# Performance work log

Measured on AMD Instinct MI355X. Metric: run time of the kernel, lower is better.

Reference implementation:

```python
import jax, jax.numpy as jnp
import numpy as np

H = 16  # num_heads (matches init_kwargs)
MASK_VAL = -10000.0


def setup_inputs() -> dict:
    key = jax.random.key(0)
    k1, k2, k3, k4, k5 = jax.random.split(key, 5)
    B, N, C = 2, 2048, 1024
    hidden_states = jax.random.normal(k1, (B, N, C), dtype=jnp.float32)
    encoder_hidden_states = jax.random.normal(k2, (B, N, C), dtype=jnp.float32)
    pad_mask = jax.random.bernoulli(k3, 0.1, (B, N))
    # Linear weights stored as (in, out); scaled ~Xavier so softmax isn't saturated
    W_q = jax.random.normal(k4, (C, C), dtype=jnp.float32) * (C ** -0.5)
    W_c = jax.random.normal(k5, (C, 2 * C), dtype=jnp.float32) * (C ** -0.5)
    return {"hidden_states": hidden_states,
            "encoder_hidden_states": encoder_hidden_states,
            "pad_mask": pad_mask,
            "W_q": W_q,
            "W_c": W_c}


def _split_heads(x, B, N, C):
    # (B, N, C) -> (B, H, N, D)
    return x.reshape(B, N, H, C // H).transpose(0, 2, 1, 3)


def reference(hidden_states, encoder_hidden_states, pad_mask, W_q, W_c):
    B, N, C = hidden_states.shape
    D = C // H
    scaler = D ** -0.5

    q = hidden_states @ W_q                       # (B, N, C)
    kv = encoder_hidden_states @ W_c              # (B, N, 2C)
    k, v = kv[..., :C], kv[..., C:]

    q = _split_heads(q, B, N, C)                  # (B, H, N, D)
    k = _split_heads(k, B, N, C)
    v = _split_heads(v, B, N, C)

    scores = jnp.einsum('bhid,bhjd->bhij', q, k) * scaler  # (B, H, N, N)

    # construct_mask: expanded[b,i,j] = pad_mask[b,i] OR pad_mask[b,j]
    expanded = pad_mask[:, None, :, None] | pad_mask[:, None, None, :]
    scores = jnp.where(expanded, MASK_VAL, scores)

    # max-subtract + softmax (dropout_rate=0 so dropout is identity)
    scores = scores - jax.lax.stop_gradient(scores.max(axis=-1, keepdims=True))
    att_weights = jax.nn.softmax(scores, axis=-1)

    att = jnp.einsum('bhij,bhjd->bhid', att_weights, v)   # (B, H, N, D)
    att = att.transpose(0, 2, 1, 3).reshape(B, N, C)
    return att, att_weights
```

## Files before the change

### kernel.cpp

```cpp
#include <hip/hip_runtime.h>
#include <math.h>

#define B_ 2
#define N_ 2048
#define C_ 1024
#define H_ 16
#define D_ 64

typedef __attribute__((ext_vector_type(8))) short short8v;
typedef __attribute__((ext_vector_type(4))) short short4v;
typedef __attribute__((ext_vector_type(4))) float f32x4;

static __device__ __forceinline__ short f2bf(float f) {
    union { float f; unsigned u; } v; v.f = f;
    unsigned r = v.u + 0x7FFFu + ((v.u >> 16) & 1u);
    return (short)(r >> 16);
}

static __device__ __forceinline__ void splitbf(float f, short& h, short& l) {
    union { float f; unsigned u; } v; v.f = f;
    const unsigned uh = v.u & 0xFFFF0000u;
    h = (short)(uh >> 16);
    union { unsigned u; float f; } w; w.u = uh;
    union { float f; unsigned u; } x; x.f = f - w.f;
    l = (short)(x.u >> 16);
}

static __device__ __forceinline__ void lds_barrier() {
    __builtin_amdgcn_sched_barrier(0);
    asm volatile("s_waitcnt lgkmcnt(0)" ::: "memory");
    __builtin_amdgcn_s_barrier();
    __builtin_amdgcn_sched_barrier(0);
}

__global__ __launch_bounds__(256) void split_aw(const float* __restrict__ src,
                                                short* __restrict__ hi,
                                                short* __restrict__ lo,
                                                int nA,
                                                const float* __restrict__ Wm,
                                                short* __restrict__ th,
                                                short* __restrict__ tl,
                                                int K, int N) {
    __shared__ float Ls[64][68];
    const int t = threadIdx.x;
    if ((int)blockIdx.x < nA) {
        const int i = (blockIdx.x * 256 + t) * 4;
        const float4 f = *(const float4*)&src[i];
        short4v h, l;
        short th_, tl_;
        splitbf(f.x, th_, tl_); h[0] = th_; l[0] = tl_;
        splitbf(f.y, th_, tl_); h[1] = th_; l[1] = tl_;
        splitbf(f.z, th_, tl_); h[2] = th_; l[2] = tl_;
        splitbf(f.w, th_, tl_); h[3] = th_; l[3] = tl_;
        *(short4v*)&hi[i] = h;
        *(short4v*)&lo[i] = l;
        return;
    }
    const int wb  = blockIdx.x - nA;
    const int nbx = N / 64;
    const int n0 = (wb % nbx) * 64;
    const int k0 = (wb / nbx) * 64;
#pragma unroll
    for (int it = 0; it < 4; ++it) {
        const int kl = it * 16 + (t >> 4);
        const int nl = (t & 15) * 4;
        *(float4*)&Ls[kl][nl] = *(const float4*)&Wm[(size_t)(k0 + kl) * N + n0 + nl];
    }
    __syncthreads();
#pragma unroll
    for (int it = 0; it < 4; ++it) {
        const int idx = it * 256 + t;
        const int nl  = idx & 63;
        const int ks  = (idx >> 6) * 4;
        short4v h, l;
#pragma unroll
        for (int j = 0; j < 4; ++j) {
            short th_, tl_;
            splitbf(Ls[ks + j][nl], th_, tl_);
            h[j] = th_; l[j] = tl_;
        }
        *(short4v*)&th[(size_t)(n0 + nl) * K + k0 + ks] = h;
        *(short4v*)&tl[(size_t)(n0 + nl) * K + k0 + ks] = l;
    }
}

#define GKSTR 40

__global__ __launch_bounds__(256) void gemm_bf3(const short* __restrict__ Ah,
                                                const short* __restrict__ Al,
                                                const short* __restrict__ Bth,
                                                const short* __restrict__ Btl,
                                                short* __restrict__ Cm,
                                                int K, int N) {
    __shared__ __align__(16) short Ahs[128][GKSTR];
    __shared__ __align__(16) short Als[128][GKSTR];
    __shared__ __align__(16) short Bhs[128][GKSTR];
    __shared__ __align__(16) short Bls[128][GKSTR];

    const int t  = threadIdx.x;
    const int w  = t >> 6;
    const int lq = t & 15;
    const int hq = (t & 63) >> 4;
    const int wr = w >> 1;
    const int wc = w & 1;
    const int m0 = blockIdx.y * 128;
    const int n0 = blockIdx.x * 128;

    const int srow = t >> 1;
    const int scol = (t & 1) * 16;

    const short* gA_h = &Ah[(size_t)(m0 + srow) * K + scol];
    const short* gA_l = &Al[(size_t)(m0 + srow) * K + scol];
    const short* gB_h = &Bth[(size_t)(n0 + srow) * K + scol];
    const short* gB_l = &Btl[(size_t)(n0 + srow) * K + scol];

    f32x4 acc[4][4];
#pragma unroll
    for (int mi = 0; mi < 4; ++mi)
#pragma unroll
        for (int ni = 0; ni < 4; ++ni) acc[mi][ni] = (f32x4){0.f, 0.f, 0.f, 0.f};

    short8v ra_h0 = *(const short8v*)gA_h,       ra_h1 = *(const short8v*)(gA_h + 8);
    short8v ra_l0 = *(const short8v*)gA_l,       ra_l1 = *(const short8v*)(gA_l + 8);
    short8v rb_h0 = *(const short8v*)gB_h,       rb_h1 = *(const short8v*)(gB_h + 8);
    short8v rb_l0 = *(const short8v*)gB_l,       rb_l1 = *(const short8v*)(gB_l + 8);

    for (int k0 = 0; k0 < K; k0 += 32) {
        __syncthreads();
        *(short8v*)&Ahs[srow][scol]     = ra_h0;
        *(short8v*)&Ahs[srow][scol + 8] = ra_h1;
        *(short8v*)&Als[srow][scol]     = ra_l0;
        *(short8v*)&Als[srow][scol + 8] = ra_l1;
        *(short8v*)&Bhs[srow][scol]     = rb_h0;
        *(short8v*)&Bhs[srow][scol + 8] = rb_h1;
        *(short8v*)&Bls[srow][scol]     = rb_l0;
        *(short8v*)&Bls[srow][scol + 8] = rb_l1;
        __syncthreads();

        const int kn = k0 + 32;
        if (kn < K) {
            ra_h0 = *(const short8v*)(gA_h + kn); ra_h1 = *(const short8v*)(gA_h + kn + 8);
            ra_l0 = *(const short8v*)(gA_l + kn); ra_l1 = *(const short8v*)(gA_l + kn + 8);
            rb_h0 = *(const short8v*)(gB_h + kn); rb_h1 = *(const short8v*)(gB_h + kn + 8);
            rb_l0 = *(const short8v*)(gB_l + kn); rb_l1 = *(const short8v*)(gB_l + kn + 8);
        }

        short8v bnh[4], bnl[4];
#pragma unroll
        for (int ni = 0; ni < 4; ++ni) {
            bnh[ni] = *(const short8v*)&Bhs[wc * 64 + ni * 16 + lq][hq * 8];
            bnl[ni] = *(const short8v*)&Bls[wc * 64 + ni * 16 + lq][hq * 8];
        }
#pragma unroll
        for (int mi = 0; mi < 4; ++mi) {
            const short8v amh = *(const short8v*)&Ahs[wr * 64 + mi * 16 + lq][hq * 8];
            const short8v aml = *(const short8v*)&Als[wr * 64 + mi * 16 + lq][hq * 8];
#pragma unroll
            for (int ni = 0; ni < 4; ++ni) {
                acc[mi][ni] = __builtin_amdgcn_mfma_f32_16x16x32_bf16(amh, bnh[ni], acc[mi][ni], 0, 0, 0);
                acc[mi][ni] = __builtin_amdgcn_mfma_f32_16x16x32_bf16(amh, bnl[ni], acc[mi][ni], 0, 0, 0);
                acc[mi][ni] = __builtin_amdgcn_mfma_f32_16x16x32_bf16(aml, bnh[ni], acc[mi][ni], 0, 0, 0);
            }
        }
    }

#pragma unroll
    for (int mi = 0; mi < 4; ++mi)
#pragma unroll
        for (int ni = 0; ni < 4; ++ni) {
            const int col = n0 + wc * 64 + ni * 16 + lq;
#pragma unroll
            for (int r = 0; r < 4; ++r) {
                const int row = m0 + wr * 64 + mi * 16 + hq * 4 + r;
                Cm[(size_t)row * N + col] = f2bf(acc[mi][ni][r]);
            }
        }
}

__global__ __launch_bounds__(256) void v_transpose(const short* __restrict__ kv_bf,
                                                   short* __restrict__ vt) {
    __shared__ __align__(16) short Ls[128][72];
    const int t  = threadIdx.x;
    const int jt = blockIdx.x * 128;
    const int h  = blockIdx.y;
    const int b  = blockIdx.z;
    const short* src = kv_bf + (size_t)b * N_ * 2 * C_ + C_ + h * D_;
#pragma unroll
    for (int it = 0; it < 4; ++it) {
        const int idx = it * 256 + t;
        const int j = idx >> 3, d0 = (idx & 7) * 8;
        *(short8v*)&Ls[j][d0] = *(const short8v*)&src[(size_t)(jt + j) * (2 * C_) + d0];
    }
    __syncthreads();
    short* dst = vt + ((size_t)(b * H_ + h)) * D_ * N_;
#pragma unroll
    for (int it = 0; it < 4; ++it) {
        const int idx = it * 256 + t;
        const int d  = idx >> 4;
        const int j0 = (idx & 15) * 8;
        short8v s;
#pragma unroll
        for (int jj = 0; jj < 8; ++jj) s[jj] = Ls[j0 + jj][d];
        *(short8v*)&dst[(size_t)d * N_ + jt + j0] = s;
    }
}

#define KSTR 72
#define VSTR 136
#define PSTR 136

__global__ __launch_bounds__(256) void attn_mfma(const short* __restrict__ q,
                                                 const short* __restrict__ kv,
                                                 const short* __restrict__ vtg,
                                                 const int* __restrict__ mask,
                                                 float* __restrict__ out_att,
                                                 float* __restrict__ out_w) {
    __shared__ __align__(16) short Ks[128][KSTR];
    __shared__ __align__(16) short Vt[64][VSTR];
    __shared__ __align__(16) short Ps[4][32][PSTR];
    __shared__ float linv_s[4][32];
    __shared__ int   mcol_s[128];

    const int t  = threadIdx.x;
    const int w  = t >> 6;
    const int l  = t & 63;
    const int lq = l & 15;
    const int hq = l >> 4;

    const int lin = blockIdx.x;
    const int swz = (lin & 7) * 64 + (lin >> 3);
    const int qb = swz & 15;
    const int h  = (swz >> 4) & 15;
    const int b  = swz >> 8;
    const int i0 = qb * 128 + w * 32;

    const int sj = t >> 3;
    const int sd = (t & 7) * 8;
    const int vd = t >> 4;
    const int vj = (t & 15) * 8;

    short8v qa[2][2];
#pragma unroll
    for (int g = 0; g < 2; ++g) {
        const short* qrow = q + ((size_t)(b * N_ + i0 + g * 16 + lq)) * C_ + h * D_;
        qa[g][0] = *(const short8v*)&qrow[hq * 8];
        qa[g][1] = *(const short8v*)&qrow[32 + hq * 8];
    }

    int mr[2][4];
#pragma unroll
    for (int g = 0; g < 2; ++g)
#pragma unroll
        for (int r = 0; r < 4; ++r) mr[g][r] = mask[b * N_ + i0 + g * 16 + hq * 4 + r];

    const short* kbase = kv + (size_t)b * N_ * 2 * C_ + h * D_;
    const short* vtb   = vtg + ((size_t)(b * H_ + h)) * D_ * N_;

    float lsum[2][4];
#pragma unroll
    for (int g = 0; g < 2; ++g)
#pragma unroll
        for (int r = 0; r < 4; ++r) lsum[g][r] = 0.f;

    short8v kr[4];
    int mpre = 0;
#pragma unroll
    for (int it = 0; it < 4; ++it)
        kr[it] = *(const short8v*)&kbase[(size_t)(it * 32 + sj) * (2 * C_) + sd];
    if (t < 128) mpre = mask[b * N_ + t];

    for (int tile = 0; tile < 16; ++tile) {
        lds_barrier();
#pragma unroll
        for (int it = 0; it < 4; ++it)
            *(short8v*)&Ks[it * 32 + sj][sd] = kr[it];
        if (t < 128) mcol_s[t] = mpre;
        lds_barrier();

        if (tile < 15) {
            const int jn = (tile + 1) * 128;
#pragma unroll
            for (int it = 0; it < 4; ++it)
                kr[it] = *(const short8v*)&kbase[(size_t)(jn + it * 32 + sj) * (2 * C_) + sd];
            if (t < 128) mpre = mask[b * N_ + jn + t];
        }

#pragma unroll
        for (int cb = 0; cb < 8; ++cb) {
            const short8v b0 = *(short8v*)&Ks[cb * 16 + lq][hq * 8];
            const short8v b1 = *(short8v*)&Ks[cb * 16 + lq][32 + hq * 8];
            const int mc = mcol_s[cb * 16 + lq];
#pragma unroll
            for (int g = 0; g < 2; ++g) {
                f32x4 acc = {0.f, 0.f, 0.f, 0.f};
                acc = __builtin_amdgcn_mfma_f32_16x16x32_bf16(qa[g][0], b0, acc, 0, 0, 0);
                acc = __builtin_amdgcn_mfma_f32_16x16x32_bf16(qa[g][1], b1, acc, 0, 0, 0);
#pragma unroll
                for (int r = 0; r < 4; ++r)
                    lsum[g][r] += mr[g][r] ? 1.0f : (mc ? 0.0f : __expf(acc[r] * 0.125f));
            }
        }
    }
    float inv[2][4];
#pragma unroll
    for (int g = 0; g < 2; ++g)
#pragma unroll
        for (int r = 0; r < 4; ++r) {
            float s = lsum[g][r];
#pragma unroll
            for (int off = 1; off < 16; off <<= 1) s += __shfl_xor(s, off, 64);
            inv[g][r] = 1.0f / s;
        }
    if (lq == 0)
#pragma unroll
        for (int g = 0; g < 2; ++g)
#pragma unroll
            for (int r = 0; r < 4; ++r) linv_s[w][g * 16 + hq * 4 + r] = inv[g][r];

    float* wbase[2];
#pragma unroll
    for (int g = 0; g < 2; ++g)
        wbase[g] = out_w + ((size_t)((b * H_ + h) * N_ + i0 + g * 16 + hq * 4)) * N_;

    f32x4 oacc[4][2];
#pragma unroll
    for (int db = 0; db < 4; ++db)
#pragma unroll
        for (int g = 0; g < 2; ++g) oacc[db][g] = (f32x4){0.f, 0.f, 0.f, 0.f};

    short8v vr[4];
#pragma unroll
    for (int it = 0; it < 4; ++it) {
        kr[it] = *(const short8v*)&kbase[(size_t)(it * 32 + sj) * (2 * C_) + sd];
        vr[it] = *(const short8v*)&vtb[(size_t)(it * 16 + vd) * N_ + vj];
    }
    if (t < 128) mpre = mask[b * N_ + t];

    for (int tile = 0; tile < 16; ++tile) {
        const int jt = tile * 128;
        lds_barrier();
#pragma unroll
        for (int it = 0; it < 4; ++it) {
            *(short8v*)&Ks[it * 32 + sj][sd] = kr[it];
            *(short8v*)&Vt[it * 16 + vd][vj] = vr[it];
        }
        if (t < 128) mcol_s[t] = mpre;
        lds_barrier();

        if (tile < 15) {
            const int jn = jt + 128;
#pragma unroll
            for (int it = 0; it < 4; ++it) {
                kr[it] = *(const short8v*)&kbase[(size_t)(jn + it * 32 + sj) * (2 * C_) + sd];
                vr[it] = *(const short8v*)&vtb[(size_t)(it * 16 + vd) * N_ + jn + vj];
            }
            if (t < 128) mpre = mask[b * N_ + jn + t];
        }

#pragma unroll
        for (int cb = 0; cb < 8; ++cb) {
            const short8v b0 = *(short8v*)&Ks[cb * 16 + lq][hq * 8];
            const short8v b1 = *(short8v*)&Ks[cb * 16 + lq][32 + hq * 8];
            const int mc   = mcol_s[cb * 16 + lq];
            const int jcol = cb * 16 + lq;
#pragma unroll
            for (int g = 0; g < 2; ++g) {
                f32x4 acc = {0.f, 0.f, 0.f, 0.f};
                acc = __builtin_amdgcn_mfma_f32_16x16x32_bf16(qa[g][0], b0, acc, 0, 0, 0);
                acc = __builtin_amdgcn_mfma_f32_16x16x32_bf16(qa[g][1], b1, acc, 0, 0, 0);
#pragma unroll
                for (int r = 0; r < 4; ++r) {
                    const float ev = mr[g][r] ? 1.0f : (mc ? 0.0f : __expf(acc[r] * 0.125f));
                    wbase[g][(size_t)r * N_ + jt + jcol] = ev * inv[g][r];
                    Ps[w][g * 16 + hq * 4 + r][jcol] = f2bf(ev);
                }
            }
        }

        short8v pb[2][4];
#pragma unroll
        for (int kb = 0; kb < 4; ++kb) {
            pb[0][kb] = *(short8v*)&Ps[w][lq][kb * 32 + hq * 8];
            pb[1][kb] = *(short8v*)&Ps[w][16 + lq][kb * 32 + hq * 8];
        }
#pragma unroll
        for (int db = 0; db < 4; ++db)
#pragma unroll
            for (int kb = 0; kb < 4; ++kb) {
                const short8v va = *(short8v*)&Vt[db * 16 + lq][kb * 32 + hq * 8];
                oacc[db][0] = __builtin_amdgcn_mfma_f32_16x16x32_bf16(va, pb[0][kb], oacc[db][0], 0, 0, 0);
                oacc[db][1] = __builtin_amdgcn_mfma_f32_16x16x32_bf16(va, pb[1][kb], oacc[db][1], 0, 0, 0);
            }
    }

#pragma unroll
    for (int g = 0; g < 2; ++g) {
        const float invi = linv_s[w][g * 16 + lq];
        const size_t abase = ((size_t)(b * N_ + i0 + g * 16 + lq)) * C_ + h * D_;
#pragma unroll
        for (int db = 0; db < 4; ++db)
#pragma unroll
            for (int r = 0; r < 4; ++r)
                out_att[abase + db * 16 + hq * 4 + r] = oacc[db][g][r] * invi;
    }
}

extern "C" void kernel_launch(void* const* d_in, const int* in_sizes, int n_in,
                              void* d_out, int out_size, void* d_ws, size_t ws_size,
                              hipStream_t stream) {
    const float* hs   = (const float*)d_in[0];
    const float* ehs  = (const float*)d_in[1];
    const int*   mask = (const int*)d_in[2];
    const float* W_q  = (const float*)d_in[3];
    const float* W_c  = (const float*)d_in[4];

    float* out_att = (float*)d_out;
    float* out_w   = (float*)d_out + (size_t)B_ * N_ * C_;

    const size_t M1 = (size_t)1024 * 1024;
    short* qbf  = (short*)d_ws;
    short* kvbf = qbf + 4 * M1;
    short* Ah   = kvbf + 8 * M1;
    short* Al   = Ah + 4 * M1;
    short* vt   = Ah;
    short* Wth  = Al + 4 * M1;
    short* Wtl  = Wth + 2 * M1;

    const int nAblk = (B_ * N_ * C_) / 1024;

    split_aw<<<dim3(nAblk + (C_ / 64) * (C_ / 64)), 256, 0, stream>>>(
        hs, Ah, Al, nAblk, W_q, Wth, Wtl, C_, C_);
    gemm_bf3<<<dim3(C_ / 128, (B_ * N_) / 128), 256, 0, stream>>>(
        Ah, Al, Wth, Wtl, qbf, C_, C_);

    split_aw<<<dim3(nAblk + ((2 * C_) / 64) * (C_ / 64)), 256, 0, stream>>>(
        ehs, Ah, Al, nAblk, W_c, Wth, Wtl, C_, 2 * C_);
    gemm_bf3<<<dim3((2 * C_) / 128, (B_ * N_) / 128), 256, 0, stream>>>(
        Ah, Al, Wth, Wtl, kvbf, C_, 2 * C_);

    v_transpose<<<dim3(N_ / 128, H_, B_), 256, 0, stream>>>(kvbf, vt);
    attn_mfma<<<dim3(512), 256, 0, stream>>>(
        qbf, kvbf, vt, mask, out_att, out_w);
}
```

Measured before the change: 325.9 us.

## Split attention row-sum pass into separate kernel and shrink GEMM N-tile

The softmax denominator pass, previously computed inside the attention kernel before the output pass, moves to its own kernel with 1024 blocks of 16 rows per wave, writing inverse row sums to workspace that the second kernel reads. The projection GEMM tile shrinks from 128x128 to 128x64, doubling the block count to raise occupancy and wave count on the many CUs. This costs an extra launch, recomputing QK^T in both kernels as before, more global traffic for the B-tile reloads, and less register reuse per GEMM block.

```diff
diff --git a/kernel.cpp b/kernel.cpp
--- a/kernel.cpp
+++ b/kernel.cpp
@@ -94,8 +94,8 @@
                                                 int K, int N) {
     __shared__ __align__(16) short Ahs[128][GKSTR];
     __shared__ __align__(16) short Als[128][GKSTR];
-    __shared__ __align__(16) short Bhs[128][GKSTR];
-    __shared__ __align__(16) short Bls[128][GKSTR];
+    __shared__ __align__(16) short Bhs[64][GKSTR];
+    __shared__ __align__(16) short Bls[64][GKSTR];
 
     const int t  = threadIdx.x;
     const int w  = t >> 6;
@@ -104,26 +104,28 @@
     const int wr = w >> 1;
     const int wc = w & 1;
     const int m0 = blockIdx.y * 128;
-    const int n0 = blockIdx.x * 128;
+    const int n0 = blockIdx.x * 64;
 
     const int srow = t >> 1;
     const int scol = (t & 1) * 16;
+    const int brow = t >> 2;
+    const int bcol = (t & 3) * 8;
 
     const short* gA_h = &Ah[(size_t)(m0 + srow) * K + scol];
     const short* gA_l = &Al[(size_t)(m0 + srow) * K + scol];
-    const short* gB_h = &Bth[(size_t)(n0 + srow) * K + scol];
-    const short* gB_l = &Btl[(size_t)(n0 + srow) * K + scol];
-
-    f32x4 acc[4][4];
+    const short* gB_h = &Bth[(size_t)(n0 + brow) * K + bcol];
+    const short* gB_l = &Btl[(size_t)(n0 + brow) * K + bcol];
+
+    f32x4 acc[4][2];
 #pragma unroll
     for (int mi = 0; mi < 4; ++mi)
 #pragma unroll
-        for (int ni = 0; ni < 4; ++ni) acc[mi][ni] = (f32x4){0.f, 0.f, 0.f, 0.f};
-
-    short8v ra_h0 = *(const short8v*)gA_h,       ra_h1 = *(const short8v*)(gA_h + 8);
-    short8v ra_l0 = *(const short8v*)gA_l,       ra_l1 = *(const short8v*)(gA_l + 8);
-    short8v rb_h0 = *(const short8v*)gB_h,       rb_h1 = *(const short8v*)(gB_h + 8);
-    short8v rb_l0 = *(const short8v*)gB_l,       rb_l1 = *(const short8v*)(gB_l + 8);
+        for (int ni = 0; ni < 2; ++ni) acc[mi][ni] = (f32x4){0.f, 0.f, 0.f, 0.f};
+
+    short8v ra_h0 = *(const short8v*)gA_h,  ra_h1 = *(const short8v*)(gA_h + 8);
+    short8v ra_l0 = *(const short8v*)gA_l,  ra_l1 = *(const short8v*)(gA_l + 8);
+    short8v rb_h  = *(const short8v*)gB_h;
+    short8v rb_l  = *(const short8v*)gB_l;
 
     for (int k0 = 0; k0 < K; k0 += 32) {
         __syncthreads();
@@ -131,32 +133,30 @@
         *(short8v*)&Ahs[srow][scol + 8] = ra_h1;
         *(short8v*)&Als[srow][scol]     = ra_l0;
         *(short8v*)&Als[srow][scol + 8] = ra_l1;
-        *(short8v*)&Bhs[srow][scol]     = rb_h0;
-        *(short8v*)&Bhs[srow][scol + 8] = rb_h1;
-        *(short8v*)&Bls[srow][scol]     = rb_l0;
-        *(short8v*)&Bls[srow][scol + 8] = rb_l1;
+        *(short8v*)&Bhs[brow][bcol]     = rb_h;
+        *(short8v*)&Bls[brow][bcol]     = rb_l;
         __syncthreads();
 
         const int kn = k0 + 32;
         if (kn < K) {
             ra_h0 = *(const short8v*)(gA_h + kn); ra_h1 = *(const short8v*)(gA_h + kn + 8);
             ra_l0 = *(const short8v*)(gA_l + kn); ra_l1 = *(const short8v*)(gA_l + kn + 8);
-            rb_h0 = *(const short8v*)(gB_h + kn); rb_h1 = *(const short8v*)(gB_h + kn + 8);
-            rb_l0 = *(const short8v*)(gB_l + kn); rb_l1 = *(const short8v*)(gB_l + kn + 8);
-        }
-
-        short8v bnh[4], bnl[4];
-#pragma unroll
-        for (int ni = 0; ni < 4; ++ni) {
-            bnh[ni] = *(const short8v*)&Bhs[wc * 64 + ni * 16 + lq][hq * 8];
-            bnl[ni] = *(const short8v*)&Bls[wc * 64 + ni * 16 + lq][hq * 8];
+            rb_h  = *(const short8v*)(gB_h + kn);
+            rb_l  = *(const short8v*)(gB_l + kn);
+        }
+
+        short8v bnh[2], bnl[2];
+#pragma unroll
+        for (int ni = 0; ni < 2; ++ni) {
+            bnh[ni] = *(const short8v*)&Bhs[wc * 32 + ni * 16 + lq][hq * 8];
+            bnl[ni] = *(const short8v*)&Bls[wc * 32 + ni * 16 + lq][hq * 8];
         }
 #pragma unroll
         for (int mi = 0; mi < 4; ++mi) {
             const short8v amh = *(const short8v*)&Ahs[wr * 64 + mi * 16 + lq][hq * 8];
             const short8v aml = *(const short8v*)&Als[wr * 64 + mi * 16 + lq][hq * 8];
 #pragma unroll
-            for (int ni = 0; ni < 4; ++ni) {
+            for (int ni = 0; ni < 2; ++ni) {
                 acc[mi][ni] = __builtin_amdgcn_mfma_f32_16x16x32_bf16(amh, bnh[ni], acc[mi][ni], 0, 0, 0);
                 acc[mi][ni] = __builtin_amdgcn_mfma_f32_16x16x32_bf16(amh, bnl[ni], acc[mi][ni], 0, 0, 0);
                 acc[mi][ni] = __builtin_amdgcn_mfma_f32_16x16x32_bf16(aml, bnh[ni], acc[mi][ni], 0, 0, 0);
@@ -167,8 +167,8 @@
 #pragma unroll
     for (int mi = 0; mi < 4; ++mi)
 #pragma unroll
-        for (int ni = 0; ni < 4; ++ni) {
-            const int col = n0 + wc * 64 + ni * 16 + lq;
+        for (int ni = 0; ni < 2; ++ni) {
+            const int col = n0 + wc * 32 + ni * 16 + lq;
 #pragma unroll
             for (int r = 0; r < 4; ++r) {
                 const int row = m0 + wr * 64 + mi * 16 + hq * 4 + r;
@@ -209,17 +209,99 @@
 #define VSTR 136
 #define PSTR 136
 
-__global__ __launch_bounds__(256) void attn_mfma(const short* __restrict__ q,
-                                                 const short* __restrict__ kv,
-                                                 const short* __restrict__ vtg,
-                                                 const int* __restrict__ mask,
-                                                 float* __restrict__ out_att,
-                                                 float* __restrict__ out_w) {
+__global__ __launch_bounds__(256) void attn_p1(const short* __restrict__ q,
+                                               const short* __restrict__ kv,
+                                               const int* __restrict__ mask,
+                                               float* __restrict__ linv_g) {
+    __shared__ __align__(16) short Ks[128][KSTR];
+    __shared__ int mcol_s[128];
+
+    const int t  = threadIdx.x;
+    const int w  = t >> 6;
+    const int l  = t & 63;
+    const int lq = l & 15;
+    const int hq = l >> 4;
+
+    const int lin = blockIdx.x;
+    const int swz = (lin & 7) * 128 + (lin >> 3);
+    const int qb = swz & 31;
+    const int h  = (swz >> 5) & 15;
+    const int b  = swz >> 9;
+    const int i0 = qb * 64 + w * 16;
+
+    const int sj = t >> 3;
+    const int sd = (t & 7) * 8;
+
+    short8v qa[2];
+    {
+        const short* qrow = q + ((size_t)(b * N_ + i0 + lq)) * C_ + h * D_;
+        qa[0] = *(const short8v*)&qrow[hq * 8];
+        qa[1] = *(const short8v*)&qrow[32 + hq * 8];
+    }
+    int mr[4];
+#pragma unroll
+    for (int r = 0; r < 4; ++r) mr[r] = mask[b * N_ + i0 + hq * 4 + r];
+
+    const short* kbase = kv + (size_t)b * N_ * 2 * C_ + h * D_;
+
+    float lsum[4] = {0.f, 0.f, 0.f, 0.f};
+    short8v kr[4];
+    int mpre = 0;
+#pragma unroll
+    for (int it = 0; it < 4; ++it)
+        kr[it] = *(const short8v*)&kbase[(size_t)(it * 32 + sj) * (2 * C_) + sd];
+    if (t < 128) mpre = mask[b * N_ + t];
+
+    for (int tile = 0; tile < 16; ++tile) {
+        lds_barrier();
+#pragma unroll
+        for (int it = 0; it < 4; ++it)
+            *(short8v*)&Ks[it * 32 + sj][sd] = kr[it];
+        if (t < 128) mcol_s[t] = mpre;
+        lds_barrier();
+
+        if (tile < 15) {
+            const int jn = (tile + 1) * 128;
+#pragma unroll
+            for (int it = 0; it < 4; ++it)
+                kr[it] = *(const short8v*)&kbase[(size_t)(jn + it * 32 + sj) * (2 * C_) + sd];
+            if (t < 128) mpre = mask[b * N_ + jn + t];
+        }
+
+#pragma unroll
+        for (int cb = 0; cb < 8; ++cb) {
+            f32x4 acc = {0.f, 0.f, 0.f, 0.f};
+            const short8v b0 = *(short8v*)&Ks[cb * 16 + lq][hq * 8];
+            const short8v b1 = *(short8v*)&Ks[cb * 16 + lq][32 + hq * 8];
+            acc = __builtin_amdgcn_mfma_f32_16x16x32_bf16(qa[0], b0, acc, 0, 0, 0);
+            acc = __builtin_amdgcn_mfma_f32_16x16x32_bf16(qa[1], b1, acc, 0, 0, 0);
+            const int mc = mcol_s[cb * 16 + lq];
+#pragma unroll
+            for (int r = 0; r < 4; ++r)
+                lsum[r] += mr[r] ? 1.0f : (mc ? 0.0f : __expf(acc[r] * 0.125f));
+        }
+    }
+#pragma unroll
+    for (int r = 0; r < 4; ++r) {
+        float s = lsum[r];
+#pragma unroll
+        for (int off = 1; off < 16; off <<= 1) s += __shfl_xor(s, off, 64);
+        if (lq == 0)
+            linv_g[(size_t)(b * H_ + h) * N_ + i0 + hq * 4 + r] = 1.0f / s;
+    }
+}
+
+__global__ __launch_bounds__(256) void attn_p2(const short* __restrict__ q,
+                                               const short* __restrict__ kv,
+                                               const short* __restrict__ vtg,
+                                               const int* __restrict__ mask,
+                                               const float* __restrict__ linv_g,
+                                               float* __restrict__ out_att,
+                                               float* __restrict__ out_w) {
     __shared__ __align__(16) short Ks[128][KSTR];
     __shared__ __align__(16) short Vt[64][VSTR];
     __shared__ __align__(16) short Ps[4][32][PSTR];
-    __shared__ float linv_s[4][32];
-    __shared__ int   mcol_s[128];
+    __shared__ int mcol_s[128];
 
     const int t  = threadIdx.x;
     const int w  = t >> 6;
@@ -246,77 +328,22 @@
         qa[g][0] = *(const short8v*)&qrow[hq * 8];
         qa[g][1] = *(const short8v*)&qrow[32 + hq * 8];
     }
-
     int mr[2][4];
 #pragma unroll
     for (int g = 0; g < 2; ++g)
 #pragma unroll
         for (int r = 0; r < 4; ++r) mr[g][r] = mask[b * N_ + i0 + g * 16 + hq * 4 + r];
+
+    const float* lrow = linv_g + (size_t)(b * H_ + h) * N_;
+    float inv[2][4];
+#pragma unroll
+    for (int g = 0; g < 2; ++g)
+#pragma unroll
+        for (int r = 0; r < 4; ++r) inv[g][r] = lrow[i0 + g * 16 + hq * 4 + r];
 
     const short* kbase = kv + (size_t)b * N_ * 2 * C_ + h * D_;
     const short* vtb   = vtg + ((size_t)(b * H_ + h)) * D_ * N_;
 
-    float lsum[2][4];
-#pragma unroll
-    for (int g = 0; g < 2; ++g)
-#pragma unroll
-        for (int r = 0; r < 4; ++r) lsum[g][r] = 0.f;
-
-    short8v kr[4];
-    int mpre = 0;
-#pragma unroll
-    for (int it = 0; it < 4; ++it)
-        kr[it] = *(const short8v*)&kbase[(size_t)(it * 32 + sj) * (2 * C_) + sd];
-    if (t < 128) mpre = mask[b * N_ + t];
-
-    for (int tile = 0; tile < 16; ++tile) {
-        lds_barrier();
-#pragma unroll
-        for (int it = 0; it < 4; ++it)
-            *(short8v*)&Ks[it * 32 + sj][sd] = kr[it];
-        if (t < 128) mcol_s[t] = mpre;
-        lds_barrier();
-
-        if (tile < 15) {
-            const int jn = (tile + 1) * 128;
-#pragma unroll
-            for (int it = 0; it < 4; ++it)
-                kr[it] = *(const short8v*)&kbase[(size_t)(jn + it * 32 + sj) * (2 * C_) + sd];
-            if (t < 128) mpre = mask[b * N_ + jn + t];
-        }
-
-#pragma unroll
-        for (int cb = 0; cb < 8; ++cb) {
-            const short8v b0 = *(short8v*)&Ks[cb * 16 + lq][hq * 8];
-            const short8v b1 = *(short8v*)&Ks[cb * 16 + lq][32 + hq * 8];
-            const int mc = mcol_s[cb * 16 + lq];
-#pragma unroll
-            for (int g = 0; g < 2; ++g) {
-                f32x4 acc = {0.f, 0.f, 0.f, 0.f};
-                acc = __builtin_amdgcn_mfma_f32_16x16x32_bf16(qa[g][0], b0, acc, 0, 0, 0);
-                acc = __builtin_amdgcn_mfma_f32_16x16x32_bf16(qa[g][1], b1, acc, 0, 0, 0);
-#pragma unroll
-                for (int r = 0; r < 4; ++r)
-                    lsum[g][r] += mr[g][r] ? 1.0f : (mc ? 0.0f : __expf(acc[r] * 0.125f));
-            }
-        }
-    }
-    float inv[2][4];
-#pragma unroll
-    for (int g = 0; g < 2; ++g)
-#pragma unroll
-        for (int r = 0; r < 4; ++r) {
-            float s = lsum[g][r];
-#pragma unroll
-            for (int off = 1; off < 16; off <<= 1) s += __shfl_xor(s, off, 64);
-            inv[g][r] = 1.0f / s;
-        }
-    if (lq == 0)
-#pragma unroll
-        for (int g = 0; g < 2; ++g)
-#pragma unroll
-            for (int r = 0; r < 4; ++r) linv_s[w][g * 16 + hq * 4 + r] = inv[g][r];
-
     float* wbase[2];
 #pragma unroll
     for (int g = 0; g < 2; ++g)
@@ -328,7 +355,8 @@
 #pragma unroll
         for (int g = 0; g < 2; ++g) oacc[db][g] = (f32x4){0.f, 0.f, 0.f, 0.f};
 
-    short8v vr[4];
+    short8v kr[4], vr[4];
+    int mpre = 0;
 #pragma unroll
     for (int it = 0; it < 4; ++it) {
         kr[it] = *(const short8v*)&kbase[(size_t)(it * 32 + sj) * (2 * C_) + sd];
@@ -395,7 +423,7 @@
 
 #pragma unroll
     for (int g = 0; g < 2; ++g) {
-        const float invi = linv_s[w][g * 16 + lq];
+        const float invi = lrow[i0 + g * 16 + lq];
         const size_t abase = ((size_t)(b * N_ + i0 + g * 16 + lq)) * C_ + h * D_;
 #pragma unroll
         for (int db = 0; db < 4; ++db)
@@ -425,20 +453,22 @@
     short* vt   = Ah;
     short* Wth  = Al + 4 * M1;
     short* Wtl  = Wth + 2 * M1;
+    float* linv = (float*)Wth;
 
     const int nAblk = (B_ * N_ * C_) / 1024;
 
     split_aw<<<dim3(nAblk + (C_ / 64) * (C_ / 64)), 256, 0, stream>>>(
         hs, Ah, Al, nAblk, W_q, Wth, Wtl, C_, C_);
-    gemm_bf3<<<dim3(C_ / 128, (B_ * N_) / 128), 256, 0, stream>>>(
+    gemm_bf3<<<dim3(C_ / 64, (B_ * N_) / 128), 256, 0, stream>>>(
         Ah, Al, Wth, Wtl, qbf, C_, C_);
 
     split_aw<<<dim3(nAblk + ((2 * C_) / 64) * (C_ / 64)), 256, 0, stream>>>(
         ehs, Ah, Al, nAblk, W_c, Wth, Wtl, C_, 2 * C_);
-    gemm_bf3<<<dim3((2 * C_) / 128, (B_ * N_) / 128), 256, 0, stream>>>(
+    gemm_bf3<<<dim3((2 * C_) / 64, (B_ * N_) / 128), 256, 0, stream>>>(
         Ah, Al, Wth, Wtl, kvbf, C_, 2 * C_);
 
     v_transpose<<<dim3(N_ / 128, H_, B_), 256, 0, stream>>>(kvbf, vt);
-    attn_mfma<<<dim3(512), 256, 0, stream>>>(
-        qbf, kvbf, vt, mask, out_att, out_w);
-}
+    attn_p1<<<dim3(1024), 256, 0, stream>>>(qbf, kvbf, mask, linv);
+    attn_p2<<<dim3(512), 256, 0, stream>>>(
+        qbf, kvbf, vt, mask, linv, out_att, out_w);
+}
```

Measured after the change: 349.2 us. 1.07x slower.
